# Kernel tuning notes

Hardware: AMD Instinct MI355X
Metric: run time of the kernel (lower is better)

## Reference

```python
import jax, jax.numpy as jnp
import numpy as np
from jax import lax


def _lstm_cell(x, h, c, W_ih, W_hh, b_ih, b_hh):
    # PyTorch LSTMCell math, gate order: input, forget, cell(g), output
    gates = x @ W_ih.T + h @ W_hh.T + b_ih + b_hh  # [B, 4H]
    i, f, g, o = jnp.split(gates, 4, axis=-1)
    i = jax.nn.sigmoid(i)
    f = jax.nn.sigmoid(f)
    g = jnp.tanh(g)
    o = jax.nn.sigmoid(o)
    c_new = f * c + i * g
    h_new = o * jnp.tanh(c_new)
    return h_new, c_new


def setup_inputs() -> dict:
    key = jax.random.key(0)
    ks = jax.random.split(key, 9)
    T, B, D, H = 512, 64, 512, 1024
    s = 0.02  # small init scale to keep recurrence stable
    return {
        "inputs": jax.random.normal(ks[0], (T, B, D), dtype=jnp.float32),
        "W_ih0": jax.random.normal(ks[1], (4 * H, D), dtype=jnp.float32) * s,
        "W_hh0": jax.random.normal(ks[2], (4 * H, H), dtype=jnp.float32) * s,
        "b_ih0": jax.random.normal(ks[3], (4 * H,), dtype=jnp.float32) * s,
        "b_hh0": jax.random.normal(ks[4], (4 * H,), dtype=jnp.float32) * s,
        "W_ih1": jax.random.normal(ks[5], (4 * H, H), dtype=jnp.float32) * s,
        "W_hh1": jax.random.normal(ks[6], (4 * H, H), dtype=jnp.float32) * s,
        "b_ih1": jax.random.normal(ks[7], (4 * H,), dtype=jnp.float32) * s,
        "b_hh1": jax.random.normal(ks[8], (4 * H,), dtype=jnp.float32) * s,
    }


def reference(inputs, W_ih0, W_hh0, b_ih0, b_hh0, W_ih1, W_hh1, b_ih1, b_hh1):
    # 2-layer LSTM over time via lax.scan; dropout=0.0, residual=False.
    T, B, _ = inputs.shape
    H = W_hh0.shape[1]
    z = jnp.zeros((B, H), dtype=inputs.dtype)
    init = (z, z, z, z)  # (h0, c0, h1, c1)

    def step(carry, x_t):
        h0, c0, h1, c1 = carry
        h0, c0 = _lstm_cell(x_t, h0, c0, W_ih0, W_hh0, b_ih0, b_hh0)
        h1, c1 = _lstm_cell(h0, h1, c1, W_ih1, W_hh1, b_ih1, b_hh1)
        return (h0, c0, h1, c1), h1

    (h0, c0, h1, c1), outputs = lax.scan(step, init, inputs)
    # outputs: [T, B, H] from last layer; final states per layer
    return outputs, (h0, c0, h1, c1)
```

## Files before the change

kernel.cpp:

```cpp
#include <hip/hip_runtime.h>
#include <hip/hip_bf16.h>
#include <stdint.h>


#define T_STEPS 512
#define BATCH   64
#define DIN     512
#define HID     1024
#define NBLK    256
#define NTHR    512

typedef __attribute__((ext_vector_type(8)))  short short8;
typedef __attribute__((ext_vector_type(16))) float f32x16;

union U16 { unsigned long long u[2]; short8 v; };

#define OFF_WIH0 ((size_t)0)
#define OFF_WHH0 ((size_t)4194304)
#define OFF_WIH1 ((size_t)12582912)
#define OFF_WHH1 ((size_t)20971520)
#define OFF_XBF  ((size_t)29360128)
#define OFF_H0   ((size_t)62914560)
#define OFF_H1   ((size_t)(OFF_H0 + 262144))
#define OFF_CTR  ((size_t)(OFF_H1 + 262144))

__global__ void cvt_bf16x4(const float4* __restrict__ in,
                           ushort4* __restrict__ out, int n4) {
  int i = blockIdx.x * blockDim.x + threadIdx.x;
  if (i >= n4) return;
  float4 v = in[i];
  __hip_bfloat16 b0 = __float2bfloat16(v.x), b1 = __float2bfloat16(v.y),
                 b2 = __float2bfloat16(v.z), b3 = __float2bfloat16(v.w);
  ushort4 o;
  o.x = *(unsigned short*)&b0; o.y = *(unsigned short*)&b1;
  o.z = *(unsigned short*)&b2; o.w = *(unsigned short*)&b3;
  out[i] = o;
}

__device__ __forceinline__ float sigf(float x) {
  return 1.0f / (1.0f + __expf(-x));
}

__launch_bounds__(NTHR, 2)
__global__ void lstm_persist(const __hip_bfloat16* __restrict__ whh0,
                             const __hip_bfloat16* __restrict__ wih0,
                             const __hip_bfloat16* __restrict__ wih1,
                             const __hip_bfloat16* __restrict__ whh1,
                             const __hip_bfloat16* __restrict__ xbf,
                             __hip_bfloat16* h0buf, __hip_bfloat16* h1buf,
                             const float* __restrict__ bih0, const float* __restrict__ bhh0,
                             const float* __restrict__ bih1, const float* __restrict__ bhh1,
                             float* __restrict__ out, unsigned* ctr) {
  __shared__ float dump[8][2][32][32];

  const int tid = threadIdx.x;
  const int w   = tid >> 6;
  const int l   = tid & 63;
  const int cu  = blockIdx.x;
  const bool L1cu = (cu >= 128);
  const int q  = L1cu ? (cu - 128) : cu;
  const int jt = q >> 1;
  const int mh = q & 1;

  const int n    = l & 31;
  const int ksub = (l >> 5) * 8;
  const int m    = mh * 32 + n;

  const int erow = tid >> 4;
  const int ehc  = tid & 15;
  const int ecol = jt * 16 + ehc;
  const int em   = mh * 32 + erow;

  float bi, bf_, bg, bo;
  {
    const float* ba = L1cu ? bih1 : bih0;
    const float* bb = L1cu ? bhh1 : bhh0;
    bi  = ba[0 * HID + ecol] + bb[0 * HID + ecol];
    bf_ = ba[1 * HID + ecol] + bb[1 * HID + ecol];
    bg  = ba[2 * HID + ecol] + bb[2 * HID + ecol];
    bo  = ba[3 * HID + ecol] + bb[3 * HID + ecol];
  }
  float cst = 0.0f;

  const int wr0 = ((n >> 4) + 0) * HID + jt * 16 + (n & 15);
  const int wr1 = ((n >> 4) + 2) * HID + jt * 16 + (n & 15);

  short8 w1a[8], w1b[8];
  short8 w2a[8], w2b[8];
  if (!L1cu) {
#pragma unroll
    for (int kk = 0; kk < 8; ++kk) {
      int k0 = (w + 8 * kk) * 16 + ksub;
      w1a[kk] = *(const short8*)(whh0 + (size_t)wr0 * 1024 + k0);
      w1b[kk] = *(const short8*)(whh0 + (size_t)wr1 * 1024 + k0);
    }
#pragma unroll
    for (int kk = 0; kk < 4; ++kk) {
      int k0 = (w + 8 * kk) * 16 + ksub;
      w2a[kk] = *(const short8*)(wih0 + (size_t)wr0 * 512 + k0);
      w2b[kk] = *(const short8*)(wih0 + (size_t)wr1 * 512 + k0);
    }
  } else {
#pragma unroll
    for (int kk = 0; kk < 8; ++kk) {
      int k0 = (w + 8 * kk) * 16 + ksub;
      w1a[kk] = *(const short8*)(wih1 + (size_t)wr0 * 1024 + k0);
      w1b[kk] = *(const short8*)(wih1 + (size_t)wr1 * 1024 + k0);
      w2a[kk] = *(const short8*)(whh1 + (size_t)wr0 * 1024 + k0);
      w2b[kk] = *(const short8*)(whh1 + (size_t)wr1 * 1024 + k0);
    }
  }

  for (int p = 0; p <= T_STEPS; ++p) {
    const bool active = L1cu ? (p >= 1) : (p < T_STEPS);
    if (active) {
      const int pb = (p + 1) & 1;
      f32x16 acc0, acc1;
#pragma unroll
      for (int r = 0; r < 16; ++r) { acc0[r] = 0.0f; acc1[r] = 0.0f; }

      {
        const __hip_bfloat16* A1e =
            h0buf + (size_t)pb * 65536 + (size_t)m * 1024 + ksub;
        const unsigned long long* A1 = (const unsigned long long*)A1e;
        U16 a1[8];
#pragma unroll
        for (int kk = 0; kk < 8; ++kk) {
          const unsigned long long* pa = A1 + (size_t)(w + 8 * kk) * 4;
          a1[kk].u[0] = __hip_atomic_load(pa,     __ATOMIC_RELAXED, __HIP_MEMORY_SCOPE_AGENT);
          a1[kk].u[1] = __hip_atomic_load(pa + 1, __ATOMIC_RELAXED, __HIP_MEMORY_SCOPE_AGENT);
        }
#pragma unroll
        for (int kk = 0; kk < 8; ++kk) {
          acc0 = __builtin_amdgcn_mfma_f32_32x32x16_bf16(a1[kk].v, w1a[kk], acc0, 0, 0, 0);
          acc1 = __builtin_amdgcn_mfma_f32_32x32x16_bf16(a1[kk].v, w1b[kk], acc1, 0, 0, 0);
        }
      }

      if (!L1cu) {
        const short8* A2 =
            (const short8*)(xbf + ((size_t)p * 64 + m) * 512 + ksub);
        short8 a2[4];
#pragma unroll
        for (int kk = 0; kk < 4; ++kk) a2[kk] = A2[(w + 8 * kk) * 2];
#pragma unroll
        for (int kk = 0; kk < 4; ++kk) {
          acc0 = __builtin_amdgcn_mfma_f32_32x32x16_bf16(a2[kk], w2a[kk], acc0, 0, 0, 0);
          acc1 = __builtin_amdgcn_mfma_f32_32x32x16_bf16(a2[kk], w2b[kk], acc1, 0, 0, 0);
        }
      } else {
        const __hip_bfloat16* A2e =
            h1buf + (size_t)(p & 1) * 65536 + (size_t)m * 1024 + ksub;
        const unsigned long long* A2 = (const unsigned long long*)A2e;
        U16 a2[8];
#pragma unroll
        for (int kk = 0; kk < 8; ++kk) {
          const unsigned long long* pa = A2 + (size_t)(w + 8 * kk) * 4;
          a2[kk].u[0] = __hip_atomic_load(pa,     __ATOMIC_RELAXED, __HIP_MEMORY_SCOPE_AGENT);
          a2[kk].u[1] = __hip_atomic_load(pa + 1, __ATOMIC_RELAXED, __HIP_MEMORY_SCOPE_AGENT);
        }
#pragma unroll
        for (int kk = 0; kk < 8; ++kk) {
          acc0 = __builtin_amdgcn_mfma_f32_32x32x16_bf16(a2[kk].v, w2a[kk], acc0, 0, 0, 0);
          acc1 = __builtin_amdgcn_mfma_f32_32x32x16_bf16(a2[kk].v, w2b[kk], acc1, 0, 0, 0);
        }
      }

      __syncthreads();
#pragma unroll
      for (int r = 0; r < 16; ++r) {
        int row = (r & 3) + 8 * (r >> 2) + 4 * (l >> 5);
        dump[w][0][row][n] = acc0[r];
        dump[w][1][row][n] = acc1[r];
      }
      __syncthreads();

      float gi = bi, gf = bf_, gg = bg, go = bo;
#pragma unroll
      for (int ww = 0; ww < 8; ++ww) {
        gi += dump[ww][0][erow][ehc];
        gf += dump[ww][0][erow][ehc + 16];
        gg += dump[ww][1][erow][ehc];
        go += dump[ww][1][erow][ehc + 16];
      }
      float si = sigf(gi), sf = sigf(gf), so = sigf(go);
      float tg = tanhf(gg);
      cst = sf * cst + si * tg;
      float h = so * tanhf(cst);

      __hip_bfloat16 hbf = __float2bfloat16(h);
      unsigned hb = *(const unsigned short*)&hbf;
      unsigned pr = __shfl_xor(hb, 1);
      __hip_bfloat16* hdst = L1cu ? (h1buf + (size_t)((p + 1) & 1) * 65536)
                                  : (h0buf + (size_t)(p & 1) * 65536);
      if ((ehc & 1) == 0) {
        unsigned pv = hb | (pr << 16);
        __hip_atomic_store((unsigned*)(hdst + (size_t)em * 1024 + ecol), pv,
                           __ATOMIC_RELAXED, __HIP_MEMORY_SCOPE_AGENT);
      }

      if (!L1cu) {
        if (p == T_STEPS - 1) {
          out[(size_t)T_STEPS * BATCH * HID + 0 * BATCH * HID + (size_t)em * HID + ecol] = h;
          out[(size_t)T_STEPS * BATCH * HID + 1 * BATCH * HID + (size_t)em * HID + ecol] = cst;
        }
      } else {
        out[((size_t)(p - 1) * BATCH + em) * HID + ecol] = h;
        if (p == T_STEPS) {
          out[(size_t)T_STEPS * BATCH * HID + 2 * BATCH * HID + (size_t)em * HID + ecol] = h;
          out[(size_t)T_STEPS * BATCH * HID + 3 * BATCH * HID + (size_t)em * HID + ecol] = cst;
        }
      }
    }

    asm volatile("s_waitcnt vmcnt(0)" ::: "memory");
    __syncthreads();
    if (tid == 0) {
      __hip_atomic_fetch_add(ctr, 1u, __ATOMIC_RELAXED, __HIP_MEMORY_SCOPE_AGENT);
      const unsigned target = (unsigned)NBLK * (unsigned)(p + 1);
      while (__hip_atomic_load(ctr, __ATOMIC_RELAXED, __HIP_MEMORY_SCOPE_AGENT) < target)
        __builtin_amdgcn_s_sleep(1);
    }
    __syncthreads();
  }
}

extern "C" void kernel_launch(void* const* d_in, const int* in_sizes, int n_in,
                              void* d_out, int out_size, void* d_ws, size_t ws_size,
                              hipStream_t stream) {
  const float* x     = (const float*)d_in[0];
  const float* Wih0  = (const float*)d_in[1];
  const float* Whh0  = (const float*)d_in[2];
  const float* b_ih0 = (const float*)d_in[3];
  const float* b_hh0 = (const float*)d_in[4];
  const float* Wih1  = (const float*)d_in[5];
  const float* Whh1  = (const float*)d_in[6];
  const float* b_ih1 = (const float*)d_in[7];
  const float* b_hh1 = (const float*)d_in[8];
  float* out = (float*)d_out;

  char* ws = (char*)d_ws;
  __hip_bfloat16* wih0p = (__hip_bfloat16*)(ws + OFF_WIH0);
  __hip_bfloat16* whh0p = (__hip_bfloat16*)(ws + OFF_WHH0);
  __hip_bfloat16* wih1p = (__hip_bfloat16*)(ws + OFF_WIH1);
  __hip_bfloat16* whh1p = (__hip_bfloat16*)(ws + OFF_WHH1);
  __hip_bfloat16* xbfp  = (__hip_bfloat16*)(ws + OFF_XBF);
  __hip_bfloat16* h0p   = (__hip_bfloat16*)(ws + OFF_H0);
  __hip_bfloat16* h1p   = (__hip_bfloat16*)(ws + OFF_H1);
  unsigned* ctr         = (unsigned*)(ws + OFF_CTR);

  hipMemsetAsync(ws + OFF_H0, 0, 262144 * 2 + 64, stream);

  cvt_bf16x4<<<2048,  256, 0, stream>>>((const float4*)Wih0, (ushort4*)wih0p, 2097152 / 4);
  cvt_bf16x4<<<4096,  256, 0, stream>>>((const float4*)Whh0, (ushort4*)whh0p, 4194304 / 4);
  cvt_bf16x4<<<4096,  256, 0, stream>>>((const float4*)Wih1, (ushort4*)wih1p, 4194304 / 4);
  cvt_bf16x4<<<4096,  256, 0, stream>>>((const float4*)Whh1, (ushort4*)whh1p, 4194304 / 4);
  cvt_bf16x4<<<16384, 256, 0, stream>>>((const float4*)x,    (ushort4*)xbfp, 16777216 / 4);

  void* args[] = { &whh0p, &wih0p, &wih1p, &whh1p, &xbfp, &h0p, &h1p,
                   (void*)&b_ih0, (void*)&b_hh0, (void*)&b_ih1, (void*)&b_hh1,
                   &out, &ctr };
  hipLaunchCooperativeKernel((const void*)lstm_persist, dim3(NBLK), dim3(NTHR),
                             args, 0, stream);
}
```

Baseline: 7.781 ms.

## Replace global grid barrier with per-step flag counters and 8-deep hidden-state rings

```diff
diff --git a/kernel.cpp b/kernel.cpp
--- a/kernel.cpp
+++ b/kernel.cpp
@@ -4,10 +4,8 @@
 
 
 #define T_STEPS 512
-#define BATCH   64
-#define DIN     512
 #define HID     1024
-#define NBLK    256
+#define NBLK    128
 #define NTHR    512
 
 typedef __attribute__((ext_vector_type(8)))  short short8;
@@ -21,8 +19,8 @@
 #define OFF_WHH1 ((size_t)20971520)
 #define OFF_XBF  ((size_t)29360128)
 #define OFF_H0   ((size_t)62914560)
-#define OFF_H1   ((size_t)(OFF_H0 + 262144))
-#define OFF_CTR  ((size_t)(OFF_H1 + 262144))
+#define OFF_H1   ((size_t)(OFF_H0 + 1048576))
+#define OFF_CTR  ((size_t)(OFF_H1 + 1048576))
 
 __global__ void cvt_bf16x4(const float4* __restrict__ in,
                            ushort4* __restrict__ out, int n4) {
@@ -41,13 +39,20 @@
   return 1.0f / (1.0f + __expf(-x));
 }
 
+__device__ __forceinline__ void spin_ge(const unsigned* a, unsigned t) {
+  while (__hip_atomic_load(a, __ATOMIC_RELAXED, __HIP_MEMORY_SCOPE_AGENT) < t)
+    __builtin_amdgcn_s_sleep(1);
+}
+
+#define ALOAD(p)  __hip_atomic_load((p), __ATOMIC_RELAXED, __HIP_MEMORY_SCOPE_AGENT)
+
 __launch_bounds__(NTHR, 2)
 __global__ void lstm_persist(const __hip_bfloat16* __restrict__ whh0,
                              const __hip_bfloat16* __restrict__ wih0,
                              const __hip_bfloat16* __restrict__ wih1,
                              const __hip_bfloat16* __restrict__ whh1,
                              const __hip_bfloat16* __restrict__ xbf,
-                             __hip_bfloat16* h0buf, __hip_bfloat16* h1buf,
+                             __hip_bfloat16* h0ring, __hip_bfloat16* h1ring,
                              const float* __restrict__ bih0, const float* __restrict__ bhh0,
                              const float* __restrict__ bih1, const float* __restrict__ bhh1,
                              float* __restrict__ out, unsigned* ctr) {
@@ -56,20 +61,17 @@
   const int tid = threadIdx.x;
   const int w   = tid >> 6;
   const int l   = tid & 63;
-  const int cu  = blockIdx.x;
-  const bool L1cu = (cu >= 128);
-  const int q  = L1cu ? (cu - 128) : cu;
-  const int jt = q >> 1;
-  const int mh = q & 1;
+  const bool L1cu = (blockIdx.x >= 64);
+  const int jt = blockIdx.x & 63;
 
   const int n    = l & 31;
   const int ksub = (l >> 5) * 8;
-  const int m    = mh * 32 + n;
+  const bool mm2 = (w >= 4);
+  const int wq = w & 3;
 
   const int erow = tid >> 4;
   const int ehc  = tid & 15;
   const int ecol = jt * 16 + ehc;
-  const int em   = mh * 32 + erow;
 
   float bi, bf_, bg, bo;
   {
@@ -80,98 +82,86 @@
     bg  = ba[2 * HID + ecol] + bb[2 * HID + ecol];
     bo  = ba[3 * HID + ecol] + bb[3 * HID + ecol];
   }
-  float cst = 0.0f;
-
-  const int wr0 = ((n >> 4) + 0) * HID + jt * 16 + (n & 15);
-  const int wr1 = ((n >> 4) + 2) * HID + jt * 16 + (n & 15);
-
-  short8 w1a[8], w1b[8];
-  short8 w2a[8], w2b[8];
-  if (!L1cu) {
-#pragma unroll
-    for (int kk = 0; kk < 8; ++kk) {
-      int k0 = (w + 8 * kk) * 16 + ksub;
-      w1a[kk] = *(const short8*)(whh0 + (size_t)wr0 * 1024 + k0);
-      w1b[kk] = *(const short8*)(whh0 + (size_t)wr1 * 1024 + k0);
-    }
-#pragma unroll
-    for (int kk = 0; kk < 4; ++kk) {
-      int k0 = (w + 8 * kk) * 16 + ksub;
-      w2a[kk] = *(const short8*)(wih0 + (size_t)wr0 * 512 + k0);
-      w2b[kk] = *(const short8*)(wih0 + (size_t)wr1 * 512 + k0);
-    }
-  } else {
-#pragma unroll
-    for (int kk = 0; kk < 8; ++kk) {
-      int k0 = (w + 8 * kk) * 16 + ksub;
-      w1a[kk] = *(const short8*)(wih1 + (size_t)wr0 * 1024 + k0);
-      w1b[kk] = *(const short8*)(wih1 + (size_t)wr1 * 1024 + k0);
-      w2a[kk] = *(const short8*)(whh1 + (size_t)wr0 * 1024 + k0);
-      w2b[kk] = *(const short8*)(whh1 + (size_t)wr1 * 1024 + k0);
-    }
-  }
-
-  for (int p = 0; p <= T_STEPS; ++p) {
-    const bool active = L1cu ? (p >= 1) : (p < T_STEPS);
-    if (active) {
-      const int pb = (p + 1) & 1;
-      f32x16 acc0, acc1;
-#pragma unroll
-      for (int r = 0; r < 16; ++r) { acc0[r] = 0.0f; acc1[r] = 0.0f; }
-
-      {
-        const __hip_bfloat16* A1e =
-            h0buf + (size_t)pb * 65536 + (size_t)m * 1024 + ksub;
-        const unsigned long long* A1 = (const unsigned long long*)A1e;
-        U16 a1[8];
-#pragma unroll
-        for (int kk = 0; kk < 8; ++kk) {
-          const unsigned long long* pa = A1 + (size_t)(w + 8 * kk) * 4;
-          a1[kk].u[0] = __hip_atomic_load(pa,     __ATOMIC_RELAXED, __HIP_MEMORY_SCOPE_AGENT);
-          a1[kk].u[1] = __hip_atomic_load(pa + 1, __ATOMIC_RELAXED, __HIP_MEMORY_SCOPE_AGENT);
-        }
-#pragma unroll
-        for (int kk = 0; kk < 8; ++kk) {
-          acc0 = __builtin_amdgcn_mfma_f32_32x32x16_bf16(a1[kk].v, w1a[kk], acc0, 0, 0, 0);
-          acc1 = __builtin_amdgcn_mfma_f32_32x32x16_bf16(a1[kk].v, w1b[kk], acc1, 0, 0, 0);
-        }
-      }
-
-      if (!L1cu) {
-        const short8* A2 =
-            (const short8*)(xbf + ((size_t)p * 64 + m) * 512 + ksub);
-        short8 a2[4];
-#pragma unroll
-        for (int kk = 0; kk < 4; ++kk) a2[kk] = A2[(w + 8 * kk) * 2];
-#pragma unroll
-        for (int kk = 0; kk < 4; ++kk) {
-          acc0 = __builtin_amdgcn_mfma_f32_32x32x16_bf16(a2[kk], w2a[kk], acc0, 0, 0, 0);
-          acc1 = __builtin_amdgcn_mfma_f32_32x32x16_bf16(a2[kk], w2b[kk], acc1, 0, 0, 0);
-        }
-      } else {
-        const __hip_bfloat16* A2e =
-            h1buf + (size_t)(p & 1) * 65536 + (size_t)m * 1024 + ksub;
-        const unsigned long long* A2 = (const unsigned long long*)A2e;
-        U16 a2[8];
-#pragma unroll
-        for (int kk = 0; kk < 8; ++kk) {
-          const unsigned long long* pa = A2 + (size_t)(w + 8 * kk) * 4;
-          a2[kk].u[0] = __hip_atomic_load(pa,     __ATOMIC_RELAXED, __HIP_MEMORY_SCOPE_AGENT);
-          a2[kk].u[1] = __hip_atomic_load(pa + 1, __ATOMIC_RELAXED, __HIP_MEMORY_SCOPE_AGENT);
-        }
-#pragma unroll
-        for (int kk = 0; kk < 8; ++kk) {
-          acc0 = __builtin_amdgcn_mfma_f32_32x32x16_bf16(a2[kk].v, w2a[kk], acc0, 0, 0, 0);
-          acc1 = __builtin_amdgcn_mfma_f32_32x32x16_bf16(a2[kk].v, w2b[kk], acc1, 0, 0, 0);
-        }
-      }
-
+  float cst0 = 0.0f, cst1 = 0.0f;
+
+  const __hip_bfloat16* Wp = L1cu ? (mm2 ? whh1 : wih1) : (mm2 ? wih0 : whh0);
+  const int ldk = (!L1cu && mm2) ? 512 : 1024;
+  const int nkc = (!L1cu && mm2) ? 8 : 16;
+  const int r0 = (n >> 4) * HID + jt * 16 + (n & 15);
+  const int r1 = r0 + 2 * HID;
+
+  short8 wA[16], wB[16];
+#pragma unroll
+  for (int i = 0; i < 16; ++i) {
+    int ii = (i < nkc) ? i : (nkc - 1);
+    int k0 = (wq * nkc + ii) * 16 + ksub;
+    wA[i] = *(const short8*)(Wp + (size_t)r0 * ldk + k0);
+    wB[i] = *(const short8*)(Wp + (size_t)r1 * ldk + k0);
+  }
+#pragma unroll
+  for (int i = 0; i < 16; ++i) {
+    asm volatile("" : "+v"(wA[i]));
+    asm volatile("" : "+v"(wB[i]));
+  }
+
+  const int pbeg = L1cu ? 1 : 0;
+  const int pend = L1cu ? T_STEPS : (T_STEPS - 1);
+
+  for (int p = pbeg; p <= pend; ++p) {
+    if (L1cu) {
+      spin_ge(ctr + (size_t)(p - 1) * 64, 64u);
+      if (p >= 2) spin_ge(ctr + (size_t)(p - 1) * 64 + 32, 64u);
+    } else {
+      if (p >= 1) spin_ge(ctr + (size_t)(p - 1) * 64, 64u);
+      if (p >= 8) spin_ge(ctr + (size_t)(p - 7) * 64 + 32, 64u);
+    }
+
+    f32x16 a00, a01, a10, a11;
+#pragma unroll
+    for (int r = 0; r < 16; ++r) { a00[r] = 0.f; a01[r] = 0.f; a10[r] = 0.f; a11[r] = 0.f; }
+
+    if (!L1cu && mm2) {
+      const __hip_bfloat16* xb = xbf + (size_t)p * 64 * 512;
+#pragma unroll
+      for (int i = 0; i < 8; ++i) {
+        int k0 = (wq * 8 + i) * 16 + ksub;
+        short8 x0 = *(const short8*)(xb + (size_t)n * 512 + k0);
+        short8 x1 = *(const short8*)(xb + (size_t)(n + 32) * 512 + k0);
+        a00 = __builtin_amdgcn_mfma_f32_32x32x16_bf16(x0, wA[i], a00, 0, 0, 0);
+        a01 = __builtin_amdgcn_mfma_f32_32x32x16_bf16(x0, wB[i], a01, 0, 0, 0);
+        a10 = __builtin_amdgcn_mfma_f32_32x32x16_bf16(x1, wA[i], a10, 0, 0, 0);
+        a11 = __builtin_amdgcn_mfma_f32_32x32x16_bf16(x1, wB[i], a11, 0, 0, 0);
+      }
+    } else {
+      const __hip_bfloat16* hs = (!mm2)
+          ? (h0ring + (size_t)((p - 1) & 7) * 65536)
+          : (h1ring + (size_t)((p - 2) & 7) * 65536);
+#pragma unroll
+      for (int i = 0; i < 16; ++i) {
+        int k0 = (wq * 16 + i) * 16 + ksub;
+        const unsigned long long* q0 = (const unsigned long long*)(hs + (size_t)n * 1024 + k0);
+        const unsigned long long* q1 = (const unsigned long long*)(hs + (size_t)(n + 32) * 1024 + k0);
+        U16 a0v, a1v;
+        a0v.u[0] = ALOAD(q0); a0v.u[1] = ALOAD(q0 + 1);
+        a1v.u[0] = ALOAD(q1); a1v.u[1] = ALOAD(q1 + 1);
+        a00 = __builtin_amdgcn_mfma_f32_32x32x16_bf16(a0v.v, wA[i], a00, 0, 0, 0);
+        a01 = __builtin_amdgcn_mfma_f32_32x32x16_bf16(a0v.v, wB[i], a01, 0, 0, 0);
+        a10 = __builtin_amdgcn_mfma_f32_32x32x16_bf16(a1v.v, wA[i], a10, 0, 0, 0);
+        a11 = __builtin_amdgcn_mfma_f32_32x32x16_bf16(a1v.v, wB[i], a11, 0, 0, 0);
+      }
+    }
+
+    __hip_bfloat16* hdst = L1cu ? (h1ring + (size_t)((p - 1) & 7) * 65536)
+                                : (h0ring + (size_t)(p & 7) * 65536);
+    float hout[2], cout_[2];
+#pragma unroll
+    for (int rd = 0; rd < 2; ++rd) {
       __syncthreads();
 #pragma unroll
       for (int r = 0; r < 16; ++r) {
         int row = (r & 3) + 8 * (r >> 2) + 4 * (l >> 5);
-        dump[w][0][row][n] = acc0[r];
-        dump[w][1][row][n] = acc1[r];
+        dump[w][0][row][n] = rd ? a10[r] : a00[r];
+        dump[w][1][row][n] = rd ? a11[r] : a01[r];
       }
       __syncthreads();
 
@@ -185,43 +175,52 @@
       }
       float si = sigf(gi), sf = sigf(gf), so = sigf(go);
       float tg = tanhf(gg);
-      cst = sf * cst + si * tg;
-      float h = so * tanhf(cst);
+      float c  = rd ? cst1 : cst0;
+      c = sf * c + si * tg;
+      if (rd) cst1 = c; else cst0 = c;
+      float h = so * tanhf(c);
+      hout[rd] = h; cout_[rd] = c;
 
       __hip_bfloat16 hbf = __float2bfloat16(h);
       unsigned hb = *(const unsigned short*)&hbf;
       unsigned pr = __shfl_xor(hb, 1);
-      __hip_bfloat16* hdst = L1cu ? (h1buf + (size_t)((p + 1) & 1) * 65536)
-                                  : (h0buf + (size_t)(p & 1) * 65536);
       if ((ehc & 1) == 0) {
+        int em = erow + 32 * rd;
         unsigned pv = hb | (pr << 16);
         __hip_atomic_store((unsigned*)(hdst + (size_t)em * 1024 + ecol), pv,
                            __ATOMIC_RELAXED, __HIP_MEMORY_SCOPE_AGENT);
       }
-
-      if (!L1cu) {
-        if (p == T_STEPS - 1) {
-          out[(size_t)T_STEPS * BATCH * HID + 0 * BATCH * HID + (size_t)em * HID + ecol] = h;
-          out[(size_t)T_STEPS * BATCH * HID + 1 * BATCH * HID + (size_t)em * HID + ecol] = cst;
-        }
-      } else {
-        out[((size_t)(p - 1) * BATCH + em) * HID + ecol] = h;
-        if (p == T_STEPS) {
-          out[(size_t)T_STEPS * BATCH * HID + 2 * BATCH * HID + (size_t)em * HID + ecol] = h;
-          out[(size_t)T_STEPS * BATCH * HID + 3 * BATCH * HID + (size_t)em * HID + ecol] = cst;
-        }
-      }
     }
 
     asm volatile("s_waitcnt vmcnt(0)" ::: "memory");
     __syncthreads();
     if (tid == 0) {
-      __hip_atomic_fetch_add(ctr, 1u, __ATOMIC_RELAXED, __HIP_MEMORY_SCOPE_AGENT);
-      const unsigned target = (unsigned)NBLK * (unsigned)(p + 1);
-      while (__hip_atomic_load(ctr, __ATOMIC_RELAXED, __HIP_MEMORY_SCOPE_AGENT) < target)
-        __builtin_amdgcn_s_sleep(1);
-    }
-    __syncthreads();
+      unsigned* arr = L1cu ? (ctr + (size_t)p * 64 + 32) : (ctr + (size_t)p * 64);
+      __hip_atomic_fetch_add(arr, 1u, __ATOMIC_RELAXED, __HIP_MEMORY_SCOPE_AGENT);
+    }
+
+    if (L1cu) {
+#pragma unroll
+      for (int rd = 0; rd < 2; ++rd) {
+        int em = erow + 32 * rd;
+        out[((size_t)(p - 1) * 64 + em) * HID + ecol] = hout[rd];
+      }
+      if (p == T_STEPS) {
+#pragma unroll
+        for (int rd = 0; rd < 2; ++rd) {
+          int em = erow + 32 * rd;
+          out[(size_t)T_STEPS * 64 * HID + 2 * 64 * HID + (size_t)em * HID + ecol] = hout[rd];
+          out[(size_t)T_STEPS * 64 * HID + 3 * 64 * HID + (size_t)em * HID + ecol] = cout_[rd];
+        }
+      }
+    } else if (p == T_STEPS - 1) {
+#pragma unroll
+      for (int rd = 0; rd < 2; ++rd) {
+        int em = erow + 32 * rd;
+        out[(size_t)T_STEPS * 64 * HID + 0 * 64 * HID + (size_t)em * HID + ecol] = hout[rd];
+        out[(size_t)T_STEPS * 64 * HID + 1 * 64 * HID + (size_t)em * HID + ecol] = cout_[rd];
+      }
+    }
   }
 }
 
@@ -249,7 +248,7 @@
   __hip_bfloat16* h1p   = (__hip_bfloat16*)(ws + OFF_H1);
   unsigned* ctr         = (unsigned*)(ws + OFF_CTR);
 
-  hipMemsetAsync(ws + OFF_H0, 0, 262144 * 2 + 64, stream);
+  hipMemsetAsync(ws + OFF_H0, 0, 1048576 * 2 + 262144, stream);
 
   cvt_bf16x4<<<2048,  256, 0, stream>>>((const float4*)Wih0, (ushort4*)wih0p, 2097152 / 4);
   cvt_bf16x4<<<4096,  256, 0, stream>>>((const float4*)Whh0, (ushort4*)whh0p, 4194304 / 4);
```

Result: slower. 12.25 ms (+57.4%).
